# Performance work log

Measured on AMD Instinct MI355X. Metric: run time of the kernel, lower is better.

Reference implementation:

```python
import jax, jax.numpy as jnp
import numpy as np

B, T, D, NPER, E = 32, 256, 1024, 64, 65536
N = B * NPER  # total nodes
LN_EPS = 1e-5


def setup_inputs() -> dict:
    key = jax.random.key(0)
    ks = jax.random.split(key, 12)
    sc = 0.02  # init scale for weights
    inp = {
        "x": jax.random.normal(ks[0], (B, T, D), jnp.float32),
        "batch": jnp.repeat(jnp.arange(B, dtype=jnp.int32), NPER),
        "edge_index": jax.random.randint(ks[1], (2, E), 0, N, dtype=jnp.int32),
        "edge_distance_vec": jax.random.normal(ks[2], (E, 3), jnp.float32),
        "edge_distance": jax.random.uniform(ks[3], (E,), jnp.float32) + 0.5,
        "natoms": NPER,
        # energy head params: LayerNorm -> Linear(D,D) -> GELU -> Linear(D,1)
        "ln_g": jnp.ones((D,), jnp.float32),
        "ln_b": jnp.zeros((D,), jnp.float32),
        "We1": jax.random.normal(ks[4], (D, D), jnp.float32) * sc,
        "be1": jnp.zeros((D,), jnp.float32),
        "We2": jax.random.normal(ks[5], (D, 1), jnp.float32) * sc,
        "be2": jnp.zeros((1,), jnp.float32),
        # forces head params: Linear(2D,D) -> GELU -> Linear(D,1)
        "Wf1": jax.random.normal(ks[6], (2 * D, D), jnp.float32) * sc,
        "bf1": jnp.zeros((D,), jnp.float32),
        "Wf2": jax.random.normal(ks[7], (D, 1), jnp.float32) * sc,
        "bf2": jnp.zeros((1,), jnp.float32),
    }
    return inp


def reference(x, batch, edge_index, edge_distance_vec, edge_distance, natoms,
              ln_g, ln_b, We1, be1, We2, be2, Wf1, bf1, Wf2, bf2):
    # ---- energy head on CLS token ----
    cls = x[:, 0]  # [B, D]
    mu = jnp.mean(cls, axis=-1, keepdims=True)
    var = jnp.mean(jnp.square(cls - mu), axis=-1, keepdims=True)
    h = (cls - mu) / jnp.sqrt(var + LN_EPS) * ln_g + ln_b
    h = jax.nn.gelu(h @ We1 + be1, approximate=False)
    energy = h @ We2 + be2  # [B, 1]

    # ---- forces head: gather node pairs -> MLP -> scale -> scatter-sum ----
    # padded_node_mask selects tokens 1..natoms per graph; boolean indexing
    # flattens row-major, identical to this slice+reshape.
    nodes = x[:, 1:1 + natoms].reshape(-1, x.shape[-1])  # [N, D]
    ei0, ei1 = edge_index[0], edge_index[1]
    edge_inputs = jnp.concatenate([nodes[ei0], nodes[ei1]], axis=1)  # [E, 2D]
    fm = jax.nn.gelu(edge_inputs @ Wf1 + bf1, approximate=False) @ Wf2 + bf2  # [E, 1]
    force_pairs = fm * edge_distance_vec / edge_distance[:, None]  # [E, 3]
    forces = jax.ops.segment_sum(force_pairs, ei0, num_segments=batch.shape[0])  # [N, 3]
    return energy, forces
```

## Files before the change

### kernel.cpp

```cpp
#include <hip/hip_runtime.h>
#include <hip/hip_fp16.h>
#include <math.h>

#define BB 32
#define TT 256
#define DD 1024
#define NNODES 2048
#define EE 65536
#define LN_EPS 1e-5f

typedef _Float16 halfx8 __attribute__((ext_vector_type(8)));
typedef __attribute__((ext_vector_type(4))) float floatx4;

__device__ __forceinline__ float gelu_fast(float x) {
    float x2 = x * x;
    float z = x * fmaf(0.10294456f, x2, 2.30211786f);
    float e = __builtin_amdgcn_exp2f(z);
    float r = __builtin_amdgcn_rcpf(1.0f + e);
    return fmaf(-x, r, x);
}

__device__ __forceinline__ __half2 gelu_h2(__half2 x) {
    const __half2 k = __float2half2_rn(-2.4554669f);
    const __half2 one = __float2half2_rn(1.0f);
    __half2 e = h2exp2(__hmul2(x, k));
    return __hmul2(x, h2rcp(__hadd2(e, one)));
}

__device__ __forceinline__ float dot2f(__half2 a, __half2 b, float c) {
#if __has_builtin(__builtin_amdgcn_fdot2)
    typedef _Float16 v2h __attribute__((ext_vector_type(2)));
    return __builtin_amdgcn_fdot2(*(v2h*)&a, *(v2h*)&b, c, false);
#else
    float2 af = __half22float2(a), bf = __half22float2(b);
    return fmaf(af.x, bf.x, fmaf(af.y, bf.y, c));
#endif
}

__device__ __forceinline__ unsigned short f32_to_h16(float f) {
    return __half_as_ushort(__float2half_rn(f));
}

__device__ __forceinline__ void load_lds16(const void* g, void* l) {
    __builtin_amdgcn_global_load_lds(
        (const __attribute__((address_space(1))) void*)g,
        (__attribute__((address_space(3))) void*)l, 16, 0, 0);
}

__global__ __launch_bounds__(256) void k1_zero_ln_prep_kernel(
    const float* __restrict__ x, const float* __restrict__ g,
    const float* __restrict__ bta, const float* __restrict__ Wf1,
    float* __restrict__ hnorm, float* __restrict__ out,
    unsigned short* __restrict__ nodesH, unsigned short* __restrict__ Wf1T) {
    __shared__ float smem[32 * 33];
    int t = threadIdx.x;
    int b = blockIdx.x;
    if (b < BB) {
        int zi = b * 256 + t;
        if (zi < BB + NNODES * 3) out[zi] = 0.0f;
        float* red = smem;
        const float* row = x + (size_t)b * TT * DD;
        float v[4];
        float s = 0.0f;
        #pragma unroll
        for (int j = 0; j < 4; ++j) { v[j] = row[t + j * 256]; s += v[j]; }
        red[t] = s; __syncthreads();
        for (int off = 128; off > 0; off >>= 1) {
            if (t < off) red[t] += red[t + off];
            __syncthreads();
        }
        float mu = red[0] * (1.0f / DD);
        __syncthreads();
        float sq = 0.0f;
        #pragma unroll
        for (int j = 0; j < 4; ++j) { float d = v[j] - mu; sq += d * d; }
        red[t] = sq; __syncthreads();
        for (int off = 128; off > 0; off >>= 1) {
            if (t < off) red[t] += red[t + off];
            __syncthreads();
        }
        float rstd = rsqrtf(red[0] * (1.0f / DD) + LN_EPS);
        #pragma unroll
        for (int j = 0; j < 4; ++j) {
            int d = t + j * 256;
            hnorm[b * DD + d] = (v[j] - mu) * rstd * g[d] + bta[d];
        }
        return;
    }
    int pb = b - BB;
    if (pb < 2048) {
        int idx4 = (pb * 256 + t) * 4;
        int i = idx4 >> 10;
        int k = idx4 & 1023;
        const float* src = x + ((size_t)(i >> 6) * TT + 1 + (i & 63)) * DD + k;
        float4 v = *(const float4*)src;
        ushort4 o;
        o.x = f32_to_h16(v.x); o.y = f32_to_h16(v.y);
        o.z = f32_to_h16(v.z); o.w = f32_to_h16(v.w);
        *(ushort4*)&nodesH[idx4] = o;
    } else {
        int q = pb - 2048;
        float (*tile)[33] = (float(*)[33])smem;
        int tx = t & 31;
        int ty = t >> 5;
        int n0 = (q & 31) * 32;
        int kg0 = (q >> 5) * 32;
        #pragma unroll
        for (int j = 0; j < 4; ++j) {
            int r = ty * 4 + j;
            tile[r][tx] = Wf1[(size_t)(kg0 + r) * DD + n0 + tx];
        }
        __syncthreads();
        int half = kg0 >> 10;
        int kk0 = kg0 & 1023;
        unsigned short* o = Wf1T + (size_t)half * DD * DD;
        #pragma unroll
        for (int j = 0; j < 4; ++j) {
            int rn = ty * 4 + j;
            o[(size_t)(n0 + rn) * DD + kk0 + tx] = f32_to_h16(tile[tx][rn]);
        }
    }
}

__global__ __launch_bounds__(512) void k2_gemm_kernel(
    const unsigned short* __restrict__ nodesH,
    const unsigned short* __restrict__ Wf1T, const float* __restrict__ bf1,
    unsigned short* __restrict__ P, const float* __restrict__ hnorm,
    const float* __restrict__ We1, float* __restrict__ He) {
    __shared__ unsigned short smem[64 * 64 + 128 * 64];
    int t = threadIdx.x;
    int b = blockIdx.x;
    if (b < 512) {
        int sb = (b & 7) * 64 + (b >> 3);
        int half = sb >> 8;
        int n0 = (sb & 15) * 64;
        int i0 = ((sb >> 4) & 15) * 128;
        unsigned short* As = smem;
        unsigned short* Bs = smem + 64 * 64;
        int w = t >> 6;
        int lane = t & 63;
        int quad = lane >> 4;
        int l16 = lane & 15;
        int wn = (w & 1) * 32;
        int wi = (w >> 1) * 32;

        const unsigned short* Ag = Wf1T + (size_t)half * DD * DD;
        const unsigned short* Bg = nodesH;

        int sr = lane >> 3;
        int sc = (lane & 7) ^ sr;
        size_t aoff = (size_t)(n0 + w * 8 + sr) * DD + sc * 8;
        size_t boff[2];
        #pragma unroll
        for (int j = 0; j < 2; ++j)
            boff[j] = (size_t)(i0 + w * 16 + j * 8 + sr) * DD + sc * 8;

        floatx4 acc[2][2];
        #pragma unroll
        for (int a = 0; a < 2; ++a)
            #pragma unroll
            for (int c = 0; c < 2; ++c) {
                acc[a][c][0] = 0.f; acc[a][c][1] = 0.f;
                acc[a][c][2] = 0.f; acc[a][c][3] = 0.f;
            }

        for (int k0 = 0; k0 < DD; k0 += 64) {
            load_lds16(Ag + aoff + k0, (void*)(As + (w * 8) * 64));
            #pragma unroll
            for (int j = 0; j < 2; ++j)
                load_lds16(Bg + boff[j] + k0, (void*)(Bs + (w * 16 + j * 8) * 64));
            __syncthreads();
            #pragma unroll
            for (int s = 0; s < 2; ++s) {
                halfx8 af[2], bfr[2];
                #pragma unroll
                for (int f = 0; f < 2; ++f) {
                    int rn = wn + f * 16 + l16;
                    af[f] = *(const halfx8*)&As[rn * 64 + ((((s << 2) | quad) ^ (rn & 7)) << 3)];
                }
                #pragma unroll
                for (int f = 0; f < 2; ++f) {
                    int ri = wi + f * 16 + l16;
                    bfr[f] = *(const halfx8*)&Bs[ri * 64 + ((((s << 2) | quad) ^ (ri & 7)) << 3)];
                }
                #pragma unroll
                for (int fa = 0; fa < 2; ++fa)
                    #pragma unroll
                    for (int fb = 0; fb < 2; ++fb)
                        acc[fa][fb] = __builtin_amdgcn_mfma_f32_16x16x32_f16(
                            af[fa], bfr[fb], acc[fa][fb], 0, 0, 0);
            }
            __syncthreads();
        }

        unsigned short* Pout = P + (size_t)half * NNODES * DD;
        #pragma unroll
        for (int fa = 0; fa < 2; ++fa) {
            int n = n0 + wn + fa * 16 + quad * 4;
            float4 badd = make_float4(0.f, 0.f, 0.f, 0.f);
            if (half == 0) badd = *(const float4*)(bf1 + n);
            #pragma unroll
            for (int fb = 0; fb < 2; ++fb) {
                int i = i0 + wi + fb * 16 + l16;
                floatx4 v = acc[fa][fb];
                ushort4 o;
                o.x = f32_to_h16(v[0] + badd.x);
                o.y = f32_to_h16(v[1] + badd.y);
                o.z = f32_to_h16(v[2] + badd.z);
                o.w = f32_to_h16(v[3] + badd.w);
                *(ushort4*)&Pout[(size_t)i * DD + n] = o;
            }
        }
        return;
    }
    {
        int q = b - 512;
        float* hs = (float*)smem;
        int col = (q & 1) * 512 + t;
        int k0 = ((q >> 1) & 15) * 64;
        int r0 = (q >> 5) * 16;
        for (int idx = t; idx < 64 * 16; idx += 512) {
            int r = idx & 15, k = idx >> 4;
            hs[idx] = hnorm[(size_t)(r0 + r) * DD + k0 + k];
        }
        __syncthreads();
        float acc[16];
        #pragma unroll
        for (int r = 0; r < 16; ++r) acc[r] = 0.0f;
        #pragma unroll 4
        for (int k = 0; k < 64; ++k) {
            float wv = We1[(size_t)(k0 + k) * DD + col];
            const float* hrow = hs + k * 16;
            #pragma unroll
            for (int j = 0; j < 4; ++j) {
                float4 h4 = *(const float4*)(hrow + j * 4);
                acc[j * 4 + 0] = fmaf(h4.x, wv, acc[j * 4 + 0]);
                acc[j * 4 + 1] = fmaf(h4.y, wv, acc[j * 4 + 1]);
                acc[j * 4 + 2] = fmaf(h4.z, wv, acc[j * 4 + 2]);
                acc[j * 4 + 3] = fmaf(h4.w, wv, acc[j * 4 + 3]);
            }
        }
        float* o = He + (size_t)((q >> 1) & 15) * 32 * DD;
        #pragma unroll
        for (int r = 0; r < 16; ++r) o[(size_t)(r0 + r) * DD + col] = acc[r];
    }
}

__global__ __launch_bounds__(256) void k3_edge_energy2_kernel(
    const unsigned short* __restrict__ P, const int* __restrict__ edge_index,
    const float* __restrict__ evec, const float* __restrict__ edist,
    const float* __restrict__ Wf2, const float* __restrict__ bf2,
    const float* __restrict__ He, const float* __restrict__ be1,
    const float* __restrict__ We2, const float* __restrict__ be2,
    float* __restrict__ out) {
    __shared__ float red[256];
    int t = threadIdx.x;
    int b = blockIdx.x;
    if (b < 4096) {
        float* forces = out + BB;
        int lane = t & 63;
        int wv = b * 4 + (t >> 6);
        int dbase = lane * 8;
        __half2 wh[8];
        #pragma unroll
        for (int s = 0; s < 2; ++s) {
            float4 a = *(const float4*)(Wf2 + s * 512 + dbase);
            float4 c = *(const float4*)(Wf2 + s * 512 + dbase + 4);
            wh[s * 4 + 0] = __floats2half2_rn(a.x, a.y);
            wh[s * 4 + 1] = __floats2half2_rn(a.z, a.w);
            wh[s * 4 + 2] = __floats2half2_rn(c.x, c.y);
            wh[s * 4 + 3] = __floats2half2_rn(c.z, c.w);
        }
        float bias2 = bf2[0];
        const unsigned short* P1 = P + (size_t)NNODES * DD;

        int i0v[4], i1v[4];
        #pragma unroll
        for (int j = 0; j < 4; ++j) {
            int e = wv + j * 16384;
            i0v[j] = __builtin_amdgcn_readfirstlane(edge_index[e]);
            i1v[j] = __builtin_amdgcn_readfirstlane(edge_index[EE + e]);
        }

        float4 buf[2][4];
        #pragma unroll
        for (int s = 0; s < 2; ++s) {
            buf[0][0 + s] = *(const float4*)(P  + (size_t)i0v[0] * DD + dbase + s * 512);
            buf[0][2 + s] = *(const float4*)(P1 + (size_t)i1v[0] * DD + dbase + s * 512);
        }
        float accs[2];
        #pragma unroll
        for (int j = 0; j < 4; ++j) {
            if (j < 3) {
                float4* nb = buf[(j + 1) & 1];
                #pragma unroll
                for (int s = 0; s < 2; ++s) {
                    nb[0 + s] = *(const float4*)(P  + (size_t)i0v[j + 1] * DD + dbase + s * 512);
                    nb[2 + s] = *(const float4*)(P1 + (size_t)i1v[j + 1] * DD + dbase + s * 512);
                }
            }
            const float4* cb = buf[j & 1];
            float acc = 0.0f;
            #pragma unroll
            for (int s = 0; s < 2; ++s) {
                const __half2* h0 = (const __half2*)&cb[s];
                const __half2* h1 = (const __half2*)&cb[2 + s];
                #pragma unroll
                for (int jj = 0; jj < 4; ++jj) {
                    __half2 hv = __hadd2(h0[jj], h1[jj]);
                    acc = dot2f(gelu_h2(hv), wh[s * 4 + jj], acc);
                }
            }
            accs[j & 1] = acc;
            if (j & 1) {
                float a0 = accs[0], a1 = accs[1];
                a0 += __shfl_xor(a0, 32, 64);
                a1 += __shfl_xor(a1, 32, 64);
                float r = (lane < 32) ? a0 : a1;
                #pragma unroll
                for (int off = 16; off > 0; off >>= 1) r += __shfl_xor(r, off, 64);
                float fm = r + bias2;
                int l5 = lane & 31;
                if (l5 < 3) {
                    int je = (lane < 32) ? (j - 1) : j;
                    int e = wv + je * 16384;
                    int i0 = (lane < 32) ? i0v[j - 1] : i0v[j];
                    float sc = fm / edist[e];
                    atomicAdd(&forces[i0 * 3 + l5], sc * evec[e * 3 + l5]);
                }
            }
        }
        return;
    }
    {
        int bb = b - 4096;
        float p = 0.0f;
        #pragma unroll
        for (int j = 0; j < 4; ++j) {
            int c = t * 4 + j;
            float s = 0.0f;
            #pragma unroll
            for (int ks = 0; ks < 16; ++ks)
                s += He[(size_t)ks * 32 * DD + bb * DD + c];
            s += be1[c];
            p += gelu_fast(s) * We2[c];
        }
        red[t] = p; __syncthreads();
        for (int off = 128; off > 0; off >>= 1) {
            if (t < off) red[t] += red[t + off];
            __syncthreads();
        }
        if (t == 0) out[bb] = red[0] + be2[0];
    }
}

extern "C" void kernel_launch(void* const* d_in, const int* in_sizes, int n_in,
                              void* d_out, int out_size, void* d_ws, size_t ws_size,
                              hipStream_t stream) {
    const float* x    = (const float*)d_in[0];
    const int* edge_index = (const int*)d_in[2];
    const float* evec = (const float*)d_in[3];
    const float* edist = (const float*)d_in[4];
    const float* ln_g = (const float*)d_in[6];
    const float* ln_b = (const float*)d_in[7];
    const float* We1  = (const float*)d_in[8];
    const float* be1  = (const float*)d_in[9];
    const float* We2  = (const float*)d_in[10];
    const float* be2  = (const float*)d_in[11];
    const float* Wf1  = (const float*)d_in[12];
    const float* bf1  = (const float*)d_in[13];
    const float* Wf2  = (const float*)d_in[14];
    const float* bf2  = (const float*)d_in[15];

    float* out = (float*)d_out;

    char* wsb = (char*)d_ws;
    unsigned short* P      = (unsigned short*)(wsb);
    float* hnorm           = (float*)(wsb + (8u << 20));
    float* He              = (float*)(wsb + (8u << 20) + (128u << 10));
    unsigned short* nodesH = (unsigned short*)(wsb + (11u << 20));
    unsigned short* Wf1T   = (unsigned short*)(wsb + (16u << 20));

    k1_zero_ln_prep_kernel<<<4128, 256, 0, stream>>>(x, ln_g, ln_b, Wf1, hnorm,
                                                     out, nodesH, Wf1T);
    k2_gemm_kernel<<<576, 512, 0, stream>>>(nodesH, Wf1T, bf1, P, hnorm, We1, He);
    k3_edge_energy2_kernel<<<4128, 256, 0, stream>>>(P, edge_index, evec, edist,
                                                     Wf2, bf2, He, be1, We2, be2,
                                                     out);
}
```

Measured before the change: 151.1 us.

## Double-buffer LDS tiles in node GEMM and widen fp16 conversion to 8 elements

The GEMM main loop now uses two LDS buffers, so the async loads for the next K tile are issued before the current tile's MFMAs run, overlapping global-to-LDS traffic with compute. The node fp16 conversion in the prep kernel handles 8 floats per thread with 16-byte stores, which halves its block count (grid shrinks by 1024). The trade-off is doubled LDS per GEMM block, which may lower occupancy. The diff also drops one of the two barriers per iteration, which may introduce a race on the buffer being overwritten.

```diff
diff --git a/kernel.cpp b/kernel.cpp
--- a/kernel.cpp
+++ b/kernel.cpp
@@ -88,18 +88,21 @@
         return;
     }
     int pb = b - BB;
-    if (pb < 2048) {
-        int idx4 = (pb * 256 + t) * 4;
-        int i = idx4 >> 10;
-        int k = idx4 & 1023;
+    if (pb < 1024) {
+        int idx8 = (pb * 256 + t) * 8;
+        int i = idx8 >> 10;
+        int k = idx8 & 1023;
         const float* src = x + ((size_t)(i >> 6) * TT + 1 + (i & 63)) * DD + k;
-        float4 v = *(const float4*)src;
-        ushort4 o;
-        o.x = f32_to_h16(v.x); o.y = f32_to_h16(v.y);
-        o.z = f32_to_h16(v.z); o.w = f32_to_h16(v.w);
-        *(ushort4*)&nodesH[idx4] = o;
+        float4 v0 = *(const float4*)src;
+        float4 v1 = *(const float4*)(src + 4);
+        union { ushort us[8]; uint4 u4; } o;
+        o.us[0] = f32_to_h16(v0.x); o.us[1] = f32_to_h16(v0.y);
+        o.us[2] = f32_to_h16(v0.z); o.us[3] = f32_to_h16(v0.w);
+        o.us[4] = f32_to_h16(v1.x); o.us[5] = f32_to_h16(v1.y);
+        o.us[6] = f32_to_h16(v1.z); o.us[7] = f32_to_h16(v1.w);
+        *(uint4*)&nodesH[idx8] = o.u4;
     } else {
-        int q = pb - 2048;
+        int q = pb - 1024;
         float (*tile)[33] = (float(*)[33])smem;
         int tx = t & 31;
         int ty = t >> 5;
@@ -127,7 +130,7 @@
     const unsigned short* __restrict__ Wf1T, const float* __restrict__ bf1,
     unsigned short* __restrict__ P, const float* __restrict__ hnorm,
     const float* __restrict__ We1, float* __restrict__ He) {
-    __shared__ unsigned short smem[64 * 64 + 128 * 64];
+    __shared__ unsigned short smem[2 * (64 * 64 + 128 * 64)];
     int t = threadIdx.x;
     int b = blockIdx.x;
     if (b < 512) {
@@ -135,8 +138,6 @@
         int half = sb >> 8;
         int n0 = (sb & 15) * 64;
         int i0 = ((sb >> 4) & 15) * 128;
-        unsigned short* As = smem;
-        unsigned short* Bs = smem + 64 * 64;
         int w = t >> 6;
         int lane = t & 63;
         int quad = lane >> 4;
@@ -164,24 +165,38 @@
                 acc[a][c][2] = 0.f; acc[a][c][3] = 0.f;
             }
 
-        for (int k0 = 0; k0 < DD; k0 += 64) {
-            load_lds16(Ag + aoff + k0, (void*)(As + (w * 8) * 64));
-            #pragma unroll
-            for (int j = 0; j < 2; ++j)
-                load_lds16(Bg + boff[j] + k0, (void*)(Bs + (w * 16 + j * 8) * 64));
-            __syncthreads();
+        const int NT = DD / 64;
+        {
+            unsigned short* As0 = smem;
+            unsigned short* Bs0 = smem + 64 * 64;
+            load_lds16(Ag + aoff, (void*)(As0 + (w * 8) * 64));
+            load_lds16(Bg + boff[0], (void*)(Bs0 + (w * 16) * 64));
+            load_lds16(Bg + boff[1], (void*)(Bs0 + (w * 16 + 8) * 64));
+        }
+        __syncthreads();
+        for (int ts = 0; ts < NT; ++ts) {
+            unsigned short* Asc = smem + (ts & 1) * 12288;
+            unsigned short* Bsc = Asc + 64 * 64;
+            if (ts + 1 < NT) {
+                unsigned short* Asn = smem + ((ts + 1) & 1) * 12288;
+                unsigned short* Bsn = Asn + 64 * 64;
+                size_t k0 = (size_t)(ts + 1) * 64;
+                load_lds16(Ag + aoff + k0, (void*)(Asn + (w * 8) * 64));
+                load_lds16(Bg + boff[0] + k0, (void*)(Bsn + (w * 16) * 64));
+                load_lds16(Bg + boff[1] + k0, (void*)(Bsn + (w * 16 + 8) * 64));
+            }
             #pragma unroll
             for (int s = 0; s < 2; ++s) {
                 halfx8 af[2], bfr[2];
                 #pragma unroll
                 for (int f = 0; f < 2; ++f) {
                     int rn = wn + f * 16 + l16;
-                    af[f] = *(const halfx8*)&As[rn * 64 + ((((s << 2) | quad) ^ (rn & 7)) << 3)];
+                    af[f] = *(const halfx8*)&Asc[rn * 64 + ((((s << 2) | quad) ^ (rn & 7)) << 3)];
                 }
                 #pragma unroll
                 for (int f = 0; f < 2; ++f) {
                     int ri = wi + f * 16 + l16;
-                    bfr[f] = *(const halfx8*)&Bs[ri * 64 + ((((s << 2) | quad) ^ (ri & 7)) << 3)];
+                    bfr[f] = *(const halfx8*)&Bsc[ri * 64 + ((((s << 2) | quad) ^ (ri & 7)) << 3)];
                 }
                 #pragma unroll
                 for (int fa = 0; fa < 2; ++fa)
@@ -381,7 +396,7 @@
     unsigned short* nodesH = (unsigned short*)(wsb + (11u << 20));
     unsigned short* Wf1T   = (unsigned short*)(wsb + (16u << 20));
 
-    k1_zero_ln_prep_kernel<<<4128, 256, 0, stream>>>(x, ln_g, ln_b, Wf1, hnorm,
+    k1_zero_ln_prep_kernel<<<3104, 256, 0, stream>>>(x, ln_g, ln_b, Wf1, hnorm,
                                                      out, nodesH, Wf1T);
     k2_gemm_kernel<<<576, 512, 0, stream>>>(nodesH, Wf1T, bf1, P, hnorm, We1, He);
     k3_edge_energy2_kernel<<<4128, 256, 0, stream>>>(P, edge_index, evec, edist,
```

Result: slower. 154.6 us (+2.3%).

## Split edge pass into two D-halves for cache-resident gathers

Applied to the files above, without the earlier changes.

The P buffer is re-laid out so each half of the hidden dimension is stored contiguously per node. The edge kernel now runs twice, once per D-half, so the gathered working set (2 x 2048 x 512 fp16 = 4MB) is more likely to stay cache-resident during each pass. The first pass writes partial dot products to a workspace buffer, and the second adds them and does the force scatter. This adds a kernel launch, a second read of the edge indices, and an extra partial-sum store and load per edge.

```diff
diff --git a/kernel.cpp b/kernel.cpp
--- a/kernel.cpp
+++ b/kernel.cpp
@@ -193,12 +193,14 @@
             __syncthreads();
         }
 
-        unsigned short* Pout = P + (size_t)half * NNODES * DD;
         #pragma unroll
         for (int fa = 0; fa < 2; ++fa) {
             int n = n0 + wn + fa * 16 + quad * 4;
             float4 badd = make_float4(0.f, 0.f, 0.f, 0.f);
             if (half == 0) badd = *(const float4*)(bf1 + n);
+            size_t dh = n >> 9;
+            size_t col = n & 511;
+            unsigned short* Pout = P + ((dh * 2 + half) * NNODES) * 512;
             #pragma unroll
             for (int fb = 0; fb < 2; ++fb) {
                 int i = i0 + wi + fb * 16 + l16;
@@ -208,7 +210,7 @@
                 o.y = f32_to_h16(v[1] + badd.y);
                 o.z = f32_to_h16(v[2] + badd.z);
                 o.w = f32_to_h16(v[3] + badd.w);
-                *(ushort4*)&Pout[(size_t)i * DD + n] = o;
+                *(ushort4*)&Pout[(size_t)i * 512 + col] = o;
             }
         }
         return;
@@ -246,13 +248,13 @@
     }
 }
 
-__global__ __launch_bounds__(256) void k3_edge_energy2_kernel(
+__global__ __launch_bounds__(256) void k3_edge_pass_kernel(
     const unsigned short* __restrict__ P, const int* __restrict__ edge_index,
     const float* __restrict__ evec, const float* __restrict__ edist,
     const float* __restrict__ Wf2, const float* __restrict__ bf2,
     const float* __restrict__ He, const float* __restrict__ be1,
     const float* __restrict__ We2, const float* __restrict__ be2,
-    float* __restrict__ out) {
+    float* __restrict__ fmpart, float* __restrict__ out, int dh) {
     __shared__ float red[256];
     int t = threadIdx.x;
     int b = blockIdx.x;
@@ -261,18 +263,18 @@
         int lane = t & 63;
         int wv = b * 4 + (t >> 6);
         int dbase = lane * 8;
-        __half2 wh[8];
-        #pragma unroll
-        for (int s = 0; s < 2; ++s) {
-            float4 a = *(const float4*)(Wf2 + s * 512 + dbase);
-            float4 c = *(const float4*)(Wf2 + s * 512 + dbase + 4);
-            wh[s * 4 + 0] = __floats2half2_rn(a.x, a.y);
-            wh[s * 4 + 1] = __floats2half2_rn(a.z, a.w);
-            wh[s * 4 + 2] = __floats2half2_rn(c.x, c.y);
-            wh[s * 4 + 3] = __floats2half2_rn(c.z, c.w);
+        __half2 wh[4];
+        {
+            float4 a = *(const float4*)(Wf2 + dh * 512 + dbase);
+            float4 c = *(const float4*)(Wf2 + dh * 512 + dbase + 4);
+            wh[0] = __floats2half2_rn(a.x, a.y);
+            wh[1] = __floats2half2_rn(a.z, a.w);
+            wh[2] = __floats2half2_rn(c.x, c.y);
+            wh[3] = __floats2half2_rn(c.z, c.w);
         }
         float bias2 = bf2[0];
-        const unsigned short* P1 = P + (size_t)NNODES * DD;
+        const unsigned short* P0h = P + (size_t)(dh * 2 + 0) * NNODES * 512;
+        const unsigned short* P1h = P + (size_t)(dh * 2 + 1) * NNODES * 512;
 
         int i0v[4], i1v[4];
         #pragma unroll
@@ -282,33 +284,25 @@
             i1v[j] = __builtin_amdgcn_readfirstlane(edge_index[EE + e]);
         }
 
-        float4 buf[2][4];
-        #pragma unroll
-        for (int s = 0; s < 2; ++s) {
-            buf[0][0 + s] = *(const float4*)(P  + (size_t)i0v[0] * DD + dbase + s * 512);
-            buf[0][2 + s] = *(const float4*)(P1 + (size_t)i1v[0] * DD + dbase + s * 512);
-        }
+        float4 buf[2][2];
+        buf[0][0] = *(const float4*)(P0h + (size_t)i0v[0] * 512 + dbase);
+        buf[0][1] = *(const float4*)(P1h + (size_t)i1v[0] * 512 + dbase);
         float accs[2];
         #pragma unroll
         for (int j = 0; j < 4; ++j) {
             if (j < 3) {
-                float4* nb = buf[(j + 1) & 1];
-                #pragma unroll
-                for (int s = 0; s < 2; ++s) {
-                    nb[0 + s] = *(const float4*)(P  + (size_t)i0v[j + 1] * DD + dbase + s * 512);
-                    nb[2 + s] = *(const float4*)(P1 + (size_t)i1v[j + 1] * DD + dbase + s * 512);
-                }
+                buf[(j + 1) & 1][0] = *(const float4*)(P0h + (size_t)i0v[j + 1] * 512 + dbase);
+                buf[(j + 1) & 1][1] = *(const float4*)(P1h + (size_t)i1v[j + 1] * 512 + dbase);
             }
             const float4* cb = buf[j & 1];
             float acc = 0.0f;
-            #pragma unroll
-            for (int s = 0; s < 2; ++s) {
-                const __half2* h0 = (const __half2*)&cb[s];
-                const __half2* h1 = (const __half2*)&cb[2 + s];
+            {
+                const __half2* h0 = (const __half2*)&cb[0];
+                const __half2* h1 = (const __half2*)&cb[1];
                 #pragma unroll
                 for (int jj = 0; jj < 4; ++jj) {
                     __half2 hv = __hadd2(h0[jj], h1[jj]);
-                    acc = dot2f(gelu_h2(hv), wh[s * 4 + jj], acc);
+                    acc = dot2f(gelu_h2(hv), wh[jj], acc);
                 }
             }
             accs[j & 1] = acc;
@@ -319,14 +313,18 @@
                 float r = (lane < 32) ? a0 : a1;
                 #pragma unroll
                 for (int off = 16; off > 0; off >>= 1) r += __shfl_xor(r, off, 64);
-                float fm = r + bias2;
-                int l5 = lane & 31;
-                if (l5 < 3) {
-                    int je = (lane < 32) ? (j - 1) : j;
-                    int e = wv + je * 16384;
-                    int i0 = (lane < 32) ? i0v[j - 1] : i0v[j];
-                    float sc = fm / edist[e];
-                    atomicAdd(&forces[i0 * 3 + l5], sc * evec[e * 3 + l5]);
+                int je = (lane < 32) ? (j - 1) : j;
+                int e = wv + je * 16384;
+                if (dh == 0) {
+                    if ((lane & 31) == 0) fmpart[e] = r;
+                } else {
+                    float fm = r + fmpart[e] + bias2;
+                    int l5 = lane & 31;
+                    if (l5 < 3) {
+                        int i0 = (lane < 32) ? i0v[j - 1] : i0v[j];
+                        float sc = fm / edist[e];
+                        atomicAdd(&forces[i0 * 3 + l5], sc * evec[e * 3 + l5]);
+                    }
                 }
             }
         }
@@ -380,11 +378,15 @@
     float* He              = (float*)(wsb + (8u << 20) + (128u << 10));
     unsigned short* nodesH = (unsigned short*)(wsb + (11u << 20));
     unsigned short* Wf1T   = (unsigned short*)(wsb + (16u << 20));
+    float* fmpart          = (float*)(wsb + (21u << 20));
 
     k1_zero_ln_prep_kernel<<<4128, 256, 0, stream>>>(x, ln_g, ln_b, Wf1, hnorm,
                                                      out, nodesH, Wf1T);
     k2_gemm_kernel<<<576, 512, 0, stream>>>(nodesH, Wf1T, bf1, P, hnorm, We1, He);
-    k3_edge_energy2_kernel<<<4128, 256, 0, stream>>>(P, edge_index, evec, edist,
-                                                     Wf2, bf2, He, be1, We2, be2,
-                                                     out);
-}
+    k3_edge_pass_kernel<<<4128, 256, 0, stream>>>(P, edge_index, evec, edist,
+                                                  Wf2, bf2, He, be1, We2, be2,
+                                                  fmpart, out, 0);
+    k3_edge_pass_kernel<<<4096, 256, 0, stream>>>(P, edge_index, evec, edist,
+                                                  Wf2, bf2, He, be1, We2, be2,
+                                                  fmpart, out, 1);
+}
```

New measurement: 150.3 us. Within noise of the previous version (-0.5%).
